# Optimization experiments

Hardware: AMD Instinct MI355X
Metric: run time of the kernel (lower is better)

## Reference

```python
import jax, jax.numpy as jnp
import numpy as np

# Complete A-ary tree of depth D, nodes stored in level order.
# Children of node i are A*i+1 .. A*i+A.
B, A, D = 512, 4, 6
N = (A**D - 1) // (A - 1)  # 1365 nodes per tree
V, E_EMB, E_ENC = 50000, 128, 128


def setup_inputs() -> dict:
    key = jax.random.key(0)
    ks = jax.random.split(key, 5)
    tokens = jax.random.randint(ks[0], (B, N), 0, V)
    emb = jax.random.normal(ks[1], (V, E_EMB), jnp.float32) * 0.02
    Wc_W = jax.random.normal(ks[2], (E_ENC, E_EMB), jnp.float32) / np.sqrt(E_EMB)
    Wc_b = jnp.zeros((E_ENC,), jnp.float32)
    Ws_W = jax.random.normal(ks[3], (E_ENC, E_ENC), jnp.float32) / np.sqrt(E_ENC)
    Ws_b = jnp.zeros((E_ENC,), jnp.float32)
    return {"tokens": tokens, "emb": emb, "Wc_W": Wc_W, "Wc_b": Wc_b,
            "Ws_W": Ws_W, "Ws_b": Ws_b, "bs": B}


def reference(tokens, emb, Wc_W, Wc_b, Ws_W, Ws_b, bs):
    # Per-node local term: W_c(embedding(token))  -> [B, N, E]
    e = emb[tokens] @ Wc_W.T + Wc_b
    level_sizes = [A ** d for d in range(D)]
    starts = np.cumsum([0] + level_sizes)  # static offsets into level order

    # Bottom-up recurrence: h(node) = e(node) + sum_children W_sum(h(child)).
    # W_sum (incl. bias) is applied per child then summed, matching the
    # per-child-slot index_copy + Linear in the original recursion.
    hs = [None] * D
    hs[D - 1] = e[:, starts[D - 1]:starts[D]]  # leaves
    for d in range(D - 2, -1, -1):
        child = hs[d + 1]                        # [B, A^(d+1), E]
        proj = child @ Ws_W.T + Ws_b             # W_sum per child
        agg = proj.reshape(bs, level_sizes[d], A, E_ENC).sum(axis=2)
        hs[d] = e[:, starts[d]:starts[d + 1]] + agg

    h_all = jnp.concatenate(hs, axis=1)          # [B, N, E]
    # node_list holds activation(h) per tree position; combine = max over nodes
    return jnp.max(jax.nn.relu(h_all), axis=1)   # [B, E]
```

## Files before the change

### kernel.cpp

```cpp
#include <hip/hip_runtime.h>
#include <hip/hip_bf16.h>

#define NTOK 1365
#define ED   128
#define STR  136
#define VROWS 50000
#define PROWS 50048

typedef __attribute__((ext_vector_type(8))) short short8;
typedef __attribute__((ext_vector_type(4))) float f32x4;

#define MFMA(a,b,c) __builtin_amdgcn_mfma_f32_16x16x32_bf16((a),(b),(c),0,0,0)

#define BAR() do {                                                   \
    __builtin_amdgcn_fence(__ATOMIC_RELEASE, "workgroup", "local");  \
    __builtin_amdgcn_s_barrier();                                    \
    __builtin_amdgcn_fence(__ATOMIC_ACQUIRE, "workgroup", "local");  \
  } while (0)

__device__ __forceinline__ ushort f2bf(float f) {
  union { float f; unsigned u; } v; v.f = f;
  unsigned r = v.u + 0x7fffu + ((v.u >> 16) & 1u);
  return (ushort)(r >> 16);
}
__device__ __forceinline__ ushort4 cvt4(float4 f) {
  ushort4 u; u.x = f2bf(f.x); u.y = f2bf(f.y); u.z = f2bf(f.z); u.w = f2bf(f.w);
  return u;
}
__device__ __forceinline__ short8 pack8(float4 a, float4 b) {
  union { ushort us[8]; short8 s8; } t;
  t.us[0]=f2bf(a.x); t.us[1]=f2bf(a.y); t.us[2]=f2bf(a.z); t.us[3]=f2bf(a.w);
  t.us[4]=f2bf(b.x); t.us[5]=f2bf(b.y); t.us[6]=f2bf(b.z); t.us[7]=f2bf(b.w);
  return t.s8;
}

__global__ __attribute__((amdgpu_flat_work_group_size(256, 256)))
void proj_kernel(const float* __restrict__ emb, const float* __restrict__ WcW,
                 const float* __restrict__ Wcb, ushort* __restrict__ P) {
  __shared__ ushort At[64 * STR];
  const int tid = threadIdx.x, w = tid >> 6, lane = tid & 63;
  const int n16 = lane & 15, quad = lane >> 4, kof = quad * 8;
  const int m0 = blockIdx.x * 64;

  #pragma unroll
  for (int i = 0; i < 8; i++) {
    const int idx = tid + i*256;
    const int r = idx >> 5, c4 = idx & 31;
    int arow = m0 + r; if (arow >= VROWS) arow = 0;
    float4 f = ((const float4*)(emb + (long)arow*ED))[c4];
    *(ushort4*)(At + r*STR + (c4 << 2)) = cvt4(f);
  }

  float bv[2];
  short8 Bp[2][4];
  #pragma unroll
  for (int j = 0; j < 2; j++) {
    const int c = w*32 + j*16 + n16;
    bv[j] = Wcb[c];
    #pragma unroll
    for (int kb = 0; kb < 4; kb++) {
      const float* pc = WcW + c*ED + kb*32 + kof;
      Bp[j][kb] = pack8(((const float4*)pc)[0], ((const float4*)pc)[1]);
    }
  }
  __syncthreads();

  #pragma unroll
  for (int i = 0; i < 4; i++) {
    f32x4 acc0 = (f32x4){0.f,0.f,0.f,0.f}, acc1 = (f32x4){0.f,0.f,0.f,0.f};
    #pragma unroll
    for (int kb = 0; kb < 4; kb++) {
      short8 a = *(const short8*)(At + (i*16 + n16)*STR + kb*32 + kof);
      acc0 = MFMA(a, Bp[0][kb], acc0);
      acc1 = MFMA(a, Bp[1][kb], acc1);
    }
    #pragma unroll
    for (int r = 0; r < 4; r++) {
      const int orow = m0 + i*16 + quad*4 + r;
      if (orow < VROWS) {
        P[(long)orow*ED + w*32 + n16]      = f2bf(acc0[r] + bv[0]);
        P[(long)orow*ED + w*32 + 16 + n16] = f2bf(acc1[r] + bv[1]);
      }
    }
  }
}

#define TKB 5472
#define SMP_BYTES (TKB + 276 * STR * 2)

__global__ __attribute__((amdgpu_flat_work_group_size(512, 512),
                          amdgpu_waves_per_eu(4, 4)))
void tree_kernel_p(
    const int* __restrict__ tokens, const ushort* __restrict__ P,
    const float* __restrict__ WsW,  const float* __restrict__ Wsb,
    float* __restrict__ out) {
  extern __shared__ char smem[];
  int*    TK  = (int*)smem;
  ushort* Xe0 = (ushort*)(smem + TKB);
  ushort* Xe1 = Xe0 + 64*STR;
  ushort* CS4 = Xe1 + 64*STR;
  ushort* CS3 = CS4 + 64*STR;
  ushort* CS2 = CS3 + 64*STR;
  ushort* CS1 = CS2 + 16*STR;
  float*  PM  = (float*)CS4;

  const int  tid = threadIdx.x;
  const int  b   = blockIdx.x;
  const int  w    = tid >> 6;
  const int  lane = tid & 63;
  const int  n16  = lane & 15;
  const int  quad = lane >> 4;
  const int  mtg  = w >> 2, ntg = w & 3;
  const int  kof  = quad * 8;

  {
    const long tokbase = (long)b * NTOK;
    for (int i = tid; i < NTOK; i += 512) TK[i] = tokens[tokbase + i];
  }

  float bsv[2];
  #pragma unroll
  for (int j = 0; j < 2; j++) bsv[j] = 4.f * Wsb[ntg*32 + j*16 + n16];

  short8 Bs[2][4];
  #pragma unroll
  for (int jt = 0; jt < 2; jt++)
    #pragma unroll
    for (int kb = 0; kb < 4; kb++) {
      const float* pc = WsW + (ntg*32 + jt*16 + n16)*ED + kb*32 + kof;
      Bs[jt][kb] = pack8(((const float4*)pc)[0], ((const float4*)pc)[1]);
    }

  short8 I2[2];
  #pragma unroll
  for (int j = 0; j < 2; j++) {
    union { ushort us[8]; short8 s8; } t;
    #pragma unroll
    for (int e = 0; e < 8; e++) t.us[e] = 0;
    if (quad == 2*j + (n16 >> 3)) t.us[n16 & 7] = 0x3F80;
    I2[j] = t.s8;
  }

  float pm[2] = {0.f, 0.f};

  short8 RA[2], RB[2];
  auto issue64 = [&](short8 (&R)[2], int ofs) {
    const int r = tid >> 3, p = tid & 7;
    const short8* src = (const short8*)(P + (long)TK[ofs + r]*ED) + (p << 1);
    R[0] = src[0]; R[1] = src[1];
  };
  auto store64 = [&](const short8 (&R)[2], ushort* Xe) {
    const int r = tid >> 3, p = tid & 7;
    short8* d = (short8*)(Xe + r*STR + (p << 4));
    d[0] = R[0]; d[1] = R[1];
  };
  auto issueN = [&](short8 (&R)[2], int ofs, int nrows) {
    const int r = tid >> 5, p = tid & 31;
    if (r < nrows) {
      ushort4 v = *((const ushort4*)(P + (long)TK[ofs + r]*ED) + p);
      R[0][0] = (short)v.x; R[0][1] = (short)v.y;
      R[0][2] = (short)v.z; R[0][3] = (short)v.w;
    }
  };
  auto storeN = [&](const short8 (&R)[2], ushort* Xe, int nrows) {
    const int r = tid >> 5, p = tid & 31;
    if (r < nrows) {
      ushort4 v; v.x = (ushort)R[0][0]; v.y = (ushort)R[0][1];
      v.z = (ushort)R[0][2]; v.w = (ushort)R[0][3];
      *(ushort4*)(Xe + r*STR + (p << 2)) = v;
    }
  };

  auto phase64 = [&](const ushort* Xe, const ushort* csrc, ushort* csdst, int csrow0) {
    f32x4 acc[2][2];
    #pragma unroll
    for (int i = 0; i < 2; i++)
      #pragma unroll
      for (int j = 0; j < 2; j++) acc[i][j] = (f32x4){0.f,0.f,0.f,0.f};
    {
      const int ko = ntg*32 + kof;
      short8 a0 = *(const short8*)(Xe + (mtg*32      + n16)*STR + ko);
      short8 a1 = *(const short8*)(Xe + (mtg*32 + 16 + n16)*STR + ko);
      acc[0][0]=MFMA(a0,I2[0],acc[0][0]); acc[0][1]=MFMA(a0,I2[1],acc[0][1]);
      acc[1][0]=MFMA(a1,I2[0],acc[1][0]); acc[1][1]=MFMA(a1,I2[1],acc[1][1]);
    }
    if (csrc) {
      #pragma unroll
      for (int kb = 0; kb < 4; kb++) {
        const int ko = kb*32 + kof;
        short8 c0 = *(const short8*)(csrc + (mtg*32      + n16)*STR + ko);
        short8 c1 = *(const short8*)(csrc + (mtg*32 + 16 + n16)*STR + ko);
        acc[0][0]=MFMA(c0,Bs[0][kb],acc[0][0]); acc[0][1]=MFMA(c0,Bs[1][kb],acc[0][1]);
        acc[1][0]=MFMA(c1,Bs[0][kb],acc[1][0]); acc[1][1]=MFMA(c1,Bs[1][kb],acc[1][1]);
      }
    }
    #pragma unroll
    for (int i = 0; i < 2; i++) {
      const int p = mtg*8 + i*4 + quad;
      #pragma unroll
      for (int j = 0; j < 2; j++) {
        const float bb = csrc ? bsv[j] : 0.f;
        f32x4 A = acc[i][j];
        float h0=A[0]+bb, h1=A[1]+bb, h2=A[2]+bb, h3=A[3]+bb;
        pm[j] = fmaxf(pm[j], fmaxf(fmaxf(h0,h1), fmaxf(h2,h3)));
        csdst[(csrow0 + p)*STR + ntg*32 + j*16 + n16] =
            f2bf(A[0]+A[1]+A[2]+A[3] + 4.f*bb);
      }
    }
  };

  auto smallphase = [&](const ushort* Xe, const ushort* csrc, int M, ushort* csdst) {
    if (mtg != 0) return;
    const int ar = (M == 16) ? n16 : ((M == 4) ? (n16 & 3) : 0);
    f32x4 acc[2];
    acc[0] = (f32x4){0.f,0.f,0.f,0.f}; acc[1] = (f32x4){0.f,0.f,0.f,0.f};
    {
      const int ko = ntg*32 + kof;
      short8 a = *(const short8*)(Xe + ar*STR + ko);
      acc[0] = MFMA(a, I2[0], acc[0]); acc[1] = MFMA(a, I2[1], acc[1]);
    }
    #pragma unroll
    for (int kb = 0; kb < 4; kb++) {
      const int ko = kb*32 + kof;
      short8 c2 = *(const short8*)(csrc + ar*STR + ko);
      acc[0] = MFMA(c2, Bs[0][kb], acc[0]); acc[1] = MFMA(c2, Bs[1][kb], acc[1]);
    }
    #pragma unroll
    for (int j = 0; j < 2; j++) {
      const float bb = bsv[j];
      f32x4 A = acc[j];
      const int c = ntg*32 + j*16 + n16;
      if (M == 16) {
        float h0=A[0]+bb, h1=A[1]+bb, h2=A[2]+bb, h3=A[3]+bb;
        pm[j] = fmaxf(pm[j], fmaxf(fmaxf(h0,h1), fmaxf(h2,h3)));
        csdst[quad*STR + c] = f2bf(A[0]+A[1]+A[2]+A[3] + 4.f*bb);
      } else if (M == 4) {
        if (quad == 0) {
          float h0=A[0]+bb, h1=A[1]+bb, h2=A[2]+bb, h3=A[3]+bb;
          pm[j] = fmaxf(pm[j], fmaxf(fmaxf(h0,h1), fmaxf(h2,h3)));
          csdst[c] = f2bf(A[0]+A[1]+A[2]+A[3] + 4.f*bb);
        }
      } else {
        if (quad == 0) pm[j] = fmaxf(pm[j], A[0] + bb);
      }
    }
  };

  __syncthreads();
  issue64(RA, 341);
  issue64(RB, 341 + 64);
  store64(RA, Xe0);
  BAR();
   issue64(RA, 341+128);     phase64(Xe0, nullptr, CS4,  0); store64(RB, Xe1); BAR();
   issue64(RB, 341+192);     phase64(Xe1, nullptr, CS4, 16); store64(RA, Xe0); BAR();
   issue64(RA, 85);          phase64(Xe0, nullptr, CS4, 32); store64(RB, Xe1); BAR();
   issue64(RB, 341+256);     phase64(Xe1, nullptr, CS4, 48); store64(RA, Xe0); BAR();
   issue64(RA, 341+256+64);  phase64(Xe0, CS4,     CS3,  0); store64(RB, Xe1); BAR();
   issue64(RB, 341+256+128); phase64(Xe1, nullptr, CS4,  0); store64(RA, Xe0); BAR();
   issue64(RA, 341+256+192); phase64(Xe0, nullptr, CS4, 16); store64(RB, Xe1); BAR();
   issue64(RB, 85+64);       phase64(Xe1, nullptr, CS4, 32); store64(RA, Xe0); BAR();
   issue64(RA, 341+512);     phase64(Xe0, nullptr, CS4, 48); store64(RB, Xe1); BAR();
   issue64(RB, 341+512+64);  phase64(Xe1, CS4,     CS3, 16); store64(RA, Xe0); BAR();
   issue64(RA, 341+512+128); phase64(Xe0, nullptr, CS4,  0); store64(RB, Xe1); BAR();
   issue64(RB, 341+512+192); phase64(Xe1, nullptr, CS4, 16); store64(RA, Xe0); BAR();
   issue64(RA, 85+128);      phase64(Xe0, nullptr, CS4, 32); store64(RB, Xe1); BAR();
   issue64(RB, 341+768);     phase64(Xe1, nullptr, CS4, 48); store64(RA, Xe0); BAR();
   issue64(RA, 341+768+64);  phase64(Xe0, CS4,     CS3, 32); store64(RB, Xe1); BAR();
   issue64(RB, 341+768+128); phase64(Xe1, nullptr, CS4,  0); store64(RA, Xe0); BAR();
   issue64(RA, 341+768+192); phase64(Xe0, nullptr, CS4, 16); store64(RB, Xe1); BAR();
   issue64(RB, 85+192);      phase64(Xe1, nullptr, CS4, 32); store64(RA, Xe0); BAR();
   issue64(RA, 21);          phase64(Xe0, nullptr, CS4, 48); store64(RB, Xe1); BAR();
   issueN(RB, 5, 16);        phase64(Xe1, CS4,     CS3, 48); store64(RA, Xe0); BAR();
  issueN(RA, 1, 4);                  phase64(Xe0, CS3,     CS2,  0);
  for (int i = tid; i < 1024; i += 512) PM[i] = 0.f;
  storeN(RB, Xe1, 16); BAR();
   issueN(RB, 0, 1);         smallphase(Xe1, CS2, 16, CS1);  storeN(RA, Xe0, 4);  BAR();
                             smallphase(Xe0, CS1, 4,  CS2);  storeN(RB, Xe1, 1);  BAR();
                             smallphase(Xe1, CS2, 1,  nullptr);

  #pragma unroll
  for (int j = 0; j < 2; j++) {
    float v = pm[j];
    v = fmaxf(v, __shfl_xor(v, 16, 64));
    v = fmaxf(v, __shfl_xor(v, 32, 64));
    if (quad == 0) PM[w*128 + ntg*32 + j*16 + n16] = v;
  }
  __syncthreads();
  if (tid < 128) {
    float m = 0.f;
    #pragma unroll
    for (int r = 0; r < 8; r++) m = fmaxf(m, PM[r*128 + tid]);
    out[(long)b*ED + tid] = m;
  }
}

#define SM_BYTES (4096 + 404 * STR * 2)

__global__ __attribute__((amdgpu_flat_work_group_size(512, 512),
                          amdgpu_waves_per_eu(2, 8)))
void tree_kernel(
    const int* __restrict__ tokens, const float* __restrict__ emb,
    const float* __restrict__ WcW,  const float* __restrict__ Wcb,
    const float* __restrict__ WsW,  const float* __restrict__ Wsb,
    float* __restrict__ out) {
  extern __shared__ char smem[];
  float*  PM  = (float*)smem;
  ushort* WsL = (ushort*)(PM + 1024);
  ushort* Xe0 = WsL + 128*STR;
  ushort* Xe1 = Xe0 + 64*STR;
  ushort* CS4 = Xe1 + 64*STR;
  ushort* CS3 = CS4 + 64*STR;
  ushort* CS2 = CS3 + 64*STR;
  ushort* CS1 = CS2 + 16*STR;

  const int  tid = threadIdx.x;
  const int  b   = blockIdx.x;
  const long tokbase = (long)b * NTOK;
  const int  w    = tid >> 6;
  const int  lane = tid & 63;
  const int  n16  = lane & 15;
  const int  quad = lane >> 4;
  const int  mtg  = w >> 2, ntg = w & 3;
  const int  kof  = quad * 8;

  float bcv[2], bsv[2];
  #pragma unroll
  for (int j = 0; j < 2; j++) {
    const int c = ntg*32 + j*16 + n16;
    bcv[j] = Wcb[c]; bsv[j] = 4.f * Wsb[c];
  }

  short8 Bc[2][4];
  #pragma unroll
  for (int jt = 0; jt < 2; jt++)
    #pragma unroll
    for (int kb = 0; kb < 4; kb++) {
      const float* pc = WcW + (ntg*32 + jt*16 + n16)*ED + kb*32 + kof;
      Bc[jt][kb] = pack8(((const float4*)pc)[0], ((const float4*)pc)[1]);
    }

  #pragma unroll
  for (int i = 0; i < 8; i++) {
    const int idx = tid + i*512;
    float4 f = ((const float4*)WsW)[idx];
    *(ushort4*)(WsL + (idx >> 5)*STR + ((idx & 31) << 2)) = cvt4(f);
  }

  for (int i = tid; i < 1024; i += 512) PM[i] = 0.f;
  float pm[2] = {0.f, 0.f};

  float4 RA[4], RB[4];
  auto issue64 = [&](float4 (&R)[4], int ofs) {
    const int r = tid >> 3, p = tid & 7;
    const float4* src = (const float4*)(emb + (long)tokens[tokbase + ofs + r]*ED) + (p << 2);
    R[0] = src[0]; R[1] = src[1]; R[2] = src[2]; R[3] = src[3];
  };
  auto store64 = [&](const float4 (&R)[4], ushort* Xe) {
    const int r = tid >> 3, p = tid & 7;
    short8* d = (short8*)(Xe + r*STR + (p << 4));
    d[0] = pack8(R[0], R[1]); d[1] = pack8(R[2], R[3]);
  };
  auto issueN = [&](float4 (&R)[4], int ofs, int nrows) {
    const int r = tid >> 5, p = tid & 31;
    if (r < nrows) R[0] = ((const float4*)(emb + (long)tokens[tokbase + ofs + r]*ED))[p];
  };
  auto storeN = [&](const float4 (&R)[4], ushort* Xe, int nrows) {
    const int r = tid >> 5, p = tid & 31;
    if (r < nrows) *(ushort4*)(Xe + r*STR + (p << 2)) = cvt4(R[0]);
  };

  auto phase64 = [&](const ushort* Xe, const ushort* csrc, ushort* csdst, int csrow0) {
    f32x4 acc[2][2];
    #pragma unroll
    for (int i = 0; i < 2; i++)
      #pragma unroll
      for (int j = 0; j < 2; j++) acc[i][j] = (f32x4){0.f,0.f,0.f,0.f};
    #pragma unroll
    for (int kb = 0; kb < 4; kb++) {
      const int ko = kb*32 + kof;
      short8 a0 = *(const short8*)(Xe + (mtg*32      + n16)*STR + ko);
      short8 a1 = *(const short8*)(Xe + (mtg*32 + 16 + n16)*STR + ko);
      acc[0][0]=MFMA(a0,Bc[0][kb],acc[0][0]); acc[0][1]=MFMA(a0,Bc[1][kb],acc[0][1]);
      acc[1][0]=MFMA(a1,Bc[0][kb],acc[1][0]); acc[1][1]=MFMA(a1,Bc[1][kb],acc[1][1]);
      if (csrc) {
        short8 c0 = *(const short8*)(csrc + (mtg*32      + n16)*STR + ko);
        short8 c1 = *(const short8*)(csrc + (mtg*32 + 16 + n16)*STR + ko);
        short8 s0 = *(const short8*)(WsL  + (ntg*32      + n16)*STR + ko);
        short8 s1 = *(const short8*)(WsL  + (ntg*32 + 16 + n16)*STR + ko);
        acc[0][0]=MFMA(c0,s0,acc[0][0]); acc[0][1]=MFMA(c0,s1,acc[0][1]);
        acc[1][0]=MFMA(c1,s0,acc[1][0]); acc[1][1]=MFMA(c1,s1,acc[1][1]);
      }
    }
    #pragma unroll
    for (int i = 0; i < 2; i++) {
      const int p = mtg*8 + i*4 + quad;
      #pragma unroll
      for (int j = 0; j < 2; j++) {
        const float bb = csrc ? (bcv[j] + bsv[j]) : bcv[j];
        f32x4 A = acc[i][j];
        float h0=A[0]+bb, h1=A[1]+bb, h2=A[2]+bb, h3=A[3]+bb;
        pm[j] = fmaxf(pm[j], fmaxf(fmaxf(h0,h1), fmaxf(h2,h3)));
        csdst[(csrow0 + p)*STR + ntg*32 + j*16 + n16] =
            f2bf(A[0]+A[1]+A[2]+A[3] + 4.f*bb);
      }
    }
  };

  auto smallphase = [&](const ushort* Xe, const ushort* csrc, int M, ushort* csdst) {
    if (mtg != 0) return;
    const int ar = (M == 16) ? n16 : ((M == 4) ? (n16 & 3) : 0);
    f32x4 acc[2];
    acc[0] = (f32x4){0.f,0.f,0.f,0.f}; acc[1] = (f32x4){0.f,0.f,0.f,0.f};
    #pragma unroll
    for (int kb = 0; kb < 4; kb++) {
      const int ko = kb*32 + kof;
      short8 a  = *(const short8*)(Xe   + ar*STR + ko);
      short8 c2 = *(const short8*)(csrc + ar*STR + ko);
      short8 s0 = *(const short8*)(WsL + (ntg*32      + n16)*STR + ko);
      short8 s1 = *(const short8*)(WsL + (ntg*32 + 16 + n16)*STR + ko);
      acc[0] = MFMA(a,  Bc[0][kb], acc[0]); acc[1] = MFMA(a,  Bc[1][kb], acc[1]);
      acc[0] = MFMA(c2, s0, acc[0]);        acc[1] = MFMA(c2, s1, acc[1]);
    }
    #pragma unroll
    for (int j = 0; j < 2; j++) {
      const float bb = bcv[j] + bsv[j];
      f32x4 A = acc[j];
      const int c = ntg*32 + j*16 + n16;
      if (M == 16) {
        float h0=A[0]+bb, h1=A[1]+bb, h2=A[2]+bb, h3=A[3]+bb;
        pm[j] = fmaxf(pm[j], fmaxf(fmaxf(h0,h1), fmaxf(h2,h3)));
        csdst[quad*STR + c] = f2bf(A[0]+A[1]+A[2]+A[3] + 4.f*bb);
      } else if (M == 4) {
        if (quad == 0) {
          float h0=A[0]+bb, h1=A[1]+bb, h2=A[2]+bb, h3=A[3]+bb;
          pm[j] = fmaxf(pm[j], fmaxf(fmaxf(h0,h1), fmaxf(h2,h3)));
          csdst[c] = f2bf(A[0]+A[1]+A[2]+A[3] + 4.f*bb);
        }
      } else {
        if (quad == 0) pm[j] = fmaxf(pm[j], A[0] + bb);
      }
    }
  };

  issue64(RA, 341);
  issue64(RB, 341 + 64);
  store64(RA, Xe0);
  __syncthreads();
  issue64(RA, 341+128);     phase64(Xe0, nullptr, CS4,  0); store64(RB, Xe1); __syncthreads();
  issue64(RB, 341+192);     phase64(Xe1, nullptr, CS4, 16); store64(RA, Xe0); __syncthreads();
  issue64(RA, 85);          phase64(Xe0, nullptr, CS4, 32); store64(RB, Xe1); __syncthreads();
  issue64(RB, 341+256);     phase64(Xe1, nullptr, CS4, 48); store64(RA, Xe0); __syncthreads();
  issue64(RA, 341+256+64);  phase64(Xe0, CS4,     CS3,  0); store64(RB, Xe1); __syncthreads();
  issue64(RB, 341+256+128); phase64(Xe1, nullptr, CS4,  0); store64(RA, Xe0); __syncthreads();
  issue64(RA, 341+256+192); phase64(Xe0, nullptr, CS4, 16); store64(RB, Xe1); __syncthreads();
  issue64(RB, 85+64);       phase64(Xe1, nullptr, CS4, 32); store64(RA, Xe0); __syncthreads();
  issue64(RA, 341+512);     phase64(Xe0, nullptr, CS4, 48); store64(RB, Xe1); __syncthreads();
  issue64(RB, 341+512+64);  phase64(Xe1, CS4,     CS3, 16); store64(RA, Xe0); __syncthreads();
  issue64(RA, 341+512+128); phase64(Xe0, nullptr, CS4,  0); store64(RB, Xe1); __syncthreads();
  issue64(RB, 341+512+192); phase64(Xe1, nullptr, CS4, 16); store64(RA, Xe0); __syncthreads();
  issue64(RA, 85+128);      phase64(Xe0, nullptr, CS4, 32); store64(RB, Xe1); __syncthreads();
  issue64(RB, 341+768);     phase64(Xe1, nullptr, CS4, 48); store64(RA, Xe0); __syncthreads();
  issue64(RA, 341+768+64);  phase64(Xe0, CS4,     CS3, 32); store64(RB, Xe1); __syncthreads();
  issue64(RB, 341+768+128); phase64(Xe1, nullptr, CS4,  0); store64(RA, Xe0); __syncthreads();
  issue64(RA, 341+768+192); phase64(Xe0, nullptr, CS4, 16); store64(RB, Xe1); __syncthreads();
  issue64(RB, 85+192);      phase64(Xe1, nullptr, CS4, 32); store64(RA, Xe0); __syncthreads();
  issue64(RA, 21);          phase64(Xe0, nullptr, CS4, 48); store64(RB, Xe1); __syncthreads();
  issueN(RB, 5, 16);        phase64(Xe1, CS4,     CS3, 48); store64(RA, Xe0); __syncthreads();
  issueN(RA, 1, 4);         phase64(Xe0, CS3,     CS2,  0); storeN(RB, Xe1, 16); __syncthreads();
  issueN(RB, 0, 1);         smallphase(Xe1, CS2, 16, CS1);  storeN(RA, Xe0, 4);  __syncthreads();
                            smallphase(Xe0, CS1, 4,  CS2);  storeN(RB, Xe1, 1);  __syncthreads();
                            smallphase(Xe1, CS2, 1,  nullptr);

  #pragma unroll
  for (int j = 0; j < 2; j++) {
    float v = pm[j];
    v = fmaxf(v, __shfl_xor(v, 16, 64));
    v = fmaxf(v, __shfl_xor(v, 32, 64));
    if (quad == 0) PM[w*128 + ntg*32 + j*16 + n16] = v;
  }
  __syncthreads();
  if (tid < 128) {
    float m = 0.f;
    #pragma unroll
    for (int r = 0; r < 8; r++) m = fmaxf(m, PM[r*128 + tid]);
    out[(long)b*ED + tid] = m;
  }
}

extern "C" void kernel_launch(void* const* d_in, const int* in_sizes, int n_in,
                              void* d_out, int out_size, void* d_ws, size_t ws_size,
                              hipStream_t stream) {
  const int*   tokens = (const int*)d_in[0];
  const float* emb    = (const float*)d_in[1];
  const float* WcW    = (const float*)d_in[2];
  const float* Wcb    = (const float*)d_in[3];
  const float* WsW    = (const float*)d_in[4];
  const float* Wsb    = (const float*)d_in[5];
  float* out = (float*)d_out;

  const size_t needP = (size_t)PROWS * ED * sizeof(ushort);
  if (d_ws != nullptr && ws_size >= needP) {
    ushort* P = (ushort*)d_ws;
    proj_kernel<<<(VROWS + 63) / 64, 256, 0, stream>>>(emb, WcW, Wcb, P);
    hipFuncSetAttribute(reinterpret_cast<const void*>(tree_kernel_p),
                        hipFuncAttributeMaxDynamicSharedMemorySize, SMP_BYTES);
    tree_kernel_p<<<512, 512, SMP_BYTES, stream>>>(tokens, P, WsW, Wsb, out);
  } else {
    hipFuncSetAttribute(reinterpret_cast<const void*>(tree_kernel),
                        hipFuncAttributeMaxDynamicSharedMemorySize, SM_BYTES);
    tree_kernel<<<512, 512, SM_BYTES, stream>>>(tokens, emb, WcW, Wcb, WsW, Wsb, out);
  }
}
```

Measured before the change: 124.8 us.

## Load embedding projections straight into MFMA fragments, dropping LDS staging

Each wave now gathers its projected-embedding rows from global memory directly into MFMA A-operand registers. Previously a cooperative load went to registers, then to double-buffered LDS tiles, then was read back per wave. This removes the two Xe LDS buffers and most per-phase barriers, keeping barriers only where the CS4/CS3 child-sum buffers are shared between phases. In exchange, the global gathers are narrower 16-byte per-lane accesses that coalesce less well, and there is less slack to hide load latency. LDS use per block also drops.

After: 127.9 us. 2.5% more time.

```diff
diff --git a/kernel.cpp b/kernel.cpp
--- a/kernel.cpp
+++ b/kernel.cpp
@@ -86,7 +86,7 @@
 }
 
 #define TKB 5472
-#define SMP_BYTES (TKB + 276 * STR * 2)
+#define SMP_BYTES (TKB + 148 * STR * 2)
 
 __global__ __attribute__((amdgpu_flat_work_group_size(512, 512),
                           amdgpu_waves_per_eu(4, 4)))
@@ -96,9 +96,7 @@
     float* __restrict__ out) {
   extern __shared__ char smem[];
   int*    TK  = (int*)smem;
-  ushort* Xe0 = (ushort*)(smem + TKB);
-  ushort* Xe1 = Xe0 + 64*STR;
-  ushort* CS4 = Xe1 + 64*STR;
+  ushort* CS4 = (ushort*)(smem + TKB);
   ushort* CS3 = CS4 + 64*STR;
   ushort* CS2 = CS3 + 64*STR;
   ushort* CS1 = CS2 + 16*STR;
@@ -143,47 +141,27 @@
 
   float pm[2] = {0.f, 0.f};
 
-  short8 RA[2], RB[2];
-  auto issue64 = [&](short8 (&R)[2], int ofs) {
-    const int r = tid >> 3, p = tid & 7;
-    const short8* src = (const short8*)(P + (long)TK[ofs + r]*ED) + (p << 1);
-    R[0] = src[0]; R[1] = src[1];
-  };
-  auto store64 = [&](const short8 (&R)[2], ushort* Xe) {
-    const int r = tid >> 3, p = tid & 7;
-    short8* d = (short8*)(Xe + r*STR + (p << 4));
-    d[0] = R[0]; d[1] = R[1];
-  };
-  auto issueN = [&](short8 (&R)[2], int ofs, int nrows) {
-    const int r = tid >> 5, p = tid & 31;
-    if (r < nrows) {
-      ushort4 v = *((const ushort4*)(P + (long)TK[ofs + r]*ED) + p);
-      R[0][0] = (short)v.x; R[0][1] = (short)v.y;
-      R[0][2] = (short)v.z; R[0][3] = (short)v.w;
-    }
-  };
-  auto storeN = [&](const short8 (&R)[2], ushort* Xe, int nrows) {
-    const int r = tid >> 5, p = tid & 31;
-    if (r < nrows) {
-      ushort4 v; v.x = (ushort)R[0][0]; v.y = (ushort)R[0][1];
-      v.z = (ushort)R[0][2]; v.w = (ushort)R[0][3];
-      *(ushort4*)(Xe + r*STR + (p << 2)) = v;
-    }
-  };
-
-  auto phase64 = [&](const ushort* Xe, const ushort* csrc, ushort* csdst, int csrow0) {
+  short8 FA[2], FB[2];
+  auto issueF = [&](short8 (&F)[2], int ofs) {
+    const int co = ntg*32 + kof;
+    F[0] = *(const short8*)(P + (long)TK[ofs + mtg*32      + n16]*ED + co);
+    F[1] = *(const short8*)(P + (long)TK[ofs + mtg*32 + 16 + n16]*ED + co);
+  };
+  auto issueS = [&](short8 (&F)[2], int ofs, int M) {
+    if (mtg != 0) return;
+    const int ar = (M == 16) ? n16 : ((M == 4) ? (n16 & 3) : 0);
+    F[0] = *(const short8*)(P + (long)TK[ofs + ar]*ED + ntg*32 + kof);
+  };
+
+  auto phase64 = [&](const short8 (&F)[2], const ushort* csrc, ushort* csdst,
+                     int csrow0) {
     f32x4 acc[2][2];
     #pragma unroll
     for (int i = 0; i < 2; i++)
       #pragma unroll
       for (int j = 0; j < 2; j++) acc[i][j] = (f32x4){0.f,0.f,0.f,0.f};
-    {
-      const int ko = ntg*32 + kof;
-      short8 a0 = *(const short8*)(Xe + (mtg*32      + n16)*STR + ko);
-      short8 a1 = *(const short8*)(Xe + (mtg*32 + 16 + n16)*STR + ko);
-      acc[0][0]=MFMA(a0,I2[0],acc[0][0]); acc[0][1]=MFMA(a0,I2[1],acc[0][1]);
-      acc[1][0]=MFMA(a1,I2[0],acc[1][0]); acc[1][1]=MFMA(a1,I2[1],acc[1][1]);
-    }
+    acc[0][0]=MFMA(F[0],I2[0],acc[0][0]); acc[0][1]=MFMA(F[0],I2[1],acc[0][1]);
+    acc[1][0]=MFMA(F[1],I2[0],acc[1][0]); acc[1][1]=MFMA(F[1],I2[1],acc[1][1]);
     if (csrc) {
       #pragma unroll
       for (int kb = 0; kb < 4; kb++) {
@@ -209,16 +187,12 @@
     }
   };
 
-  auto smallphase = [&](const ushort* Xe, const ushort* csrc, int M, ushort* csdst) {
+  auto smallphase = [&](short8 a, const ushort* csrc, int M, ushort* csdst) {
     if (mtg != 0) return;
     const int ar = (M == 16) ? n16 : ((M == 4) ? (n16 & 3) : 0);
     f32x4 acc[2];
     acc[0] = (f32x4){0.f,0.f,0.f,0.f}; acc[1] = (f32x4){0.f,0.f,0.f,0.f};
-    {
-      const int ko = ntg*32 + kof;
-      short8 a = *(const short8*)(Xe + ar*STR + ko);
-      acc[0] = MFMA(a, I2[0], acc[0]); acc[1] = MFMA(a, I2[1], acc[1]);
-    }
+    acc[0] = MFMA(a, I2[0], acc[0]); acc[1] = MFMA(a, I2[1], acc[1]);
     #pragma unroll
     for (int kb = 0; kb < 4; kb++) {
       const int ko = kb*32 + kof;
@@ -247,36 +221,33 @@
   };
 
   __syncthreads();
-  issue64(RA, 341);
-  issue64(RB, 341 + 64);
-  store64(RA, Xe0);
+  issueF(FA, 341);
+   issueF(FB, 405);  phase64(FA, nullptr, CS4,  0);
+   issueF(FA, 469);  phase64(FB, nullptr, CS4, 16);
+   issueF(FB, 533);  phase64(FA, nullptr, CS4, 32);
+   issueF(FA, 85);   phase64(FB, nullptr, CS4, 48); BAR();
+   issueF(FB, 597);   phase64(FA, CS4,     CS3,  0); BAR();
+   issueF(FA, 661);  phase64(FB, nullptr, CS4,  0);
+   issueF(FB, 725);  phase64(FA, nullptr, CS4, 16);
+   issueF(FA, 789);  phase64(FB, nullptr, CS4, 32);
+   issueF(FB, 149);  phase64(FA, nullptr, CS4, 48); BAR();
+   issueF(FA, 853);   phase64(FB, CS4,     CS3, 16); BAR();
+   issueF(FB, 917);  phase64(FA, nullptr, CS4,  0);
+   issueF(FA, 981);  phase64(FB, nullptr, CS4, 16);
+   issueF(FB, 1045); phase64(FA, nullptr, CS4, 32);
+   issueF(FA, 213);  phase64(FB, nullptr, CS4, 48); BAR();
+   issueF(FB, 1109);  phase64(FA, CS4,     CS3, 32); BAR();
+   issueF(FA, 1173); phase64(FB, nullptr, CS4,  0);
+   issueF(FB, 1237); phase64(FA, nullptr, CS4, 16);
+   issueF(FA, 1301); phase64(FB, nullptr, CS4, 32);
+   issueF(FB, 277);  phase64(FA, nullptr, CS4, 48); BAR();
+   issueF(FA, 21);    phase64(FB, CS4,     CS3, 48); BAR();
+  issueS(FB, 5, 16);                   phase64(FA, CS3,     CS2,  0);
+  for (int i = tid; i < 1024; i += 512) PM[i] = 0.f;
   BAR();
-   issue64(RA, 341+128);     phase64(Xe0, nullptr, CS4,  0); store64(RB, Xe1); BAR();
-   issue64(RB, 341+192);     phase64(Xe1, nullptr, CS4, 16); store64(RA, Xe0); BAR();
-   issue64(RA, 85);          phase64(Xe0, nullptr, CS4, 32); store64(RB, Xe1); BAR();
-   issue64(RB, 341+256);     phase64(Xe1, nullptr, CS4, 48); store64(RA, Xe0); BAR();
-   issue64(RA, 341+256+64);  phase64(Xe0, CS4,     CS3,  0); store64(RB, Xe1); BAR();
-   issue64(RB, 341+256+128); phase64(Xe1, nullptr, CS4,  0); store64(RA, Xe0); BAR();
-   issue64(RA, 341+256+192); phase64(Xe0, nullptr, CS4, 16); store64(RB, Xe1); BAR();
-   issue64(RB, 85+64);       phase64(Xe1, nullptr, CS4, 32); store64(RA, Xe0); BAR();
-   issue64(RA, 341+512);     phase64(Xe0, nullptr, CS4, 48); store64(RB, Xe1); BAR();
-   issue64(RB, 341+512+64);  phase64(Xe1, CS4,     CS3, 16); store64(RA, Xe0); BAR();
-   issue64(RA, 341+512+128); phase64(Xe0, nullptr, CS4,  0); store64(RB, Xe1); BAR();
-   issue64(RB, 341+512+192); phase64(Xe1, nullptr, CS4, 16); store64(RA, Xe0); BAR();
-   issue64(RA, 85+128);      phase64(Xe0, nullptr, CS4, 32); store64(RB, Xe1); BAR();
-   issue64(RB, 341+768);     phase64(Xe1, nullptr, CS4, 48); store64(RA, Xe0); BAR();
-   issue64(RA, 341+768+64);  phase64(Xe0, CS4,     CS3, 32); store64(RB, Xe1); BAR();
-   issue64(RB, 341+768+128); phase64(Xe1, nullptr, CS4,  0); store64(RA, Xe0); BAR();
-   issue64(RA, 341+768+192); phase64(Xe0, nullptr, CS4, 16); store64(RB, Xe1); BAR();
-   issue64(RB, 85+192);      phase64(Xe1, nullptr, CS4, 32); store64(RA, Xe0); BAR();
-   issue64(RA, 21);          phase64(Xe0, nullptr, CS4, 48); store64(RB, Xe1); BAR();
-   issueN(RB, 5, 16);        phase64(Xe1, CS4,     CS3, 48); store64(RA, Xe0); BAR();
-  issueN(RA, 1, 4);                  phase64(Xe0, CS3,     CS2,  0);
-  for (int i = tid; i < 1024; i += 512) PM[i] = 0.f;
-  storeN(RB, Xe1, 16); BAR();
-   issueN(RB, 0, 1);         smallphase(Xe1, CS2, 16, CS1);  storeN(RA, Xe0, 4);  BAR();
-                             smallphase(Xe0, CS1, 4,  CS2);  storeN(RB, Xe1, 1);  BAR();
-                             smallphase(Xe1, CS2, 1,  nullptr);
+   issueS(FA, 1, 4);   smallphase(FB[0], CS2, 16, CS1); BAR();
+   issueS(FB, 0, 1);   smallphase(FA[0], CS1, 4,  CS2); BAR();
+                       smallphase(FB[0], CS2, 1,  nullptr);
 
   #pragma unroll
   for (int j = 0; j < 2; j++) {
```
